# Kernel tuning notes

Measured on AMD Instinct MI355X. Metric: run time of the kernel, lower is better.

## Reference

```python
import jax, jax.numpy as jnp
import numpy as np

LATENT_DIM = 256
BOOK_SIZE = 8192


def setup_inputs() -> dict:
    key = jax.random.key(0)
    k1, k2 = jax.random.split(key)
    z_e = jax.random.normal(k1, (16, LATENT_DIM, 32, 32), dtype=jnp.float32)
    codebook = jax.random.normal(k2, (BOOK_SIZE, LATENT_DIM), dtype=jnp.float32)
    return {"z_e": z_e, "codebook": codebook}


def reference(z_e, codebook):
    # NCHW -> NHWC -> (B*H*W, D)
    flat_z = jnp.transpose(z_e, (0, 2, 3, 1)).reshape(-1, LATENT_DIM)
    # squared euclidean distance via matmul: ||z||^2 + ||e||^2 - 2 z.e
    dist = (
        jnp.sum(flat_z ** 2, axis=1, keepdims=True)
        + jnp.sum(codebook ** 2, axis=1)
        - 2.0 * flat_z @ codebook.T
    )  # (N, book_size)
    indices = jnp.argmin(dist, axis=1)          # (N,)
    z_q = codebook[indices]                      # (N, D) gather
    return z_q, indices
```

## Files before the change

kernel.cpp:

```cpp
#include <hip/hip_runtime.h>
#include <stdint.h>

#define NROWS 16384
#define NCODES 8192
#define DIM 256
#define EPS_S 0.4f
#define SM 0.8f

typedef __attribute__((ext_vector_type(8))) short bf16x8;
typedef __attribute__((ext_vector_type(16))) float f32x16;
typedef unsigned int uint32;

__device__ __forceinline__ unsigned short f2bf(float f) {
  union { float f; unsigned int u; } v; v.f = f;
  unsigned int u = v.u;
  return (unsigned short)((u + 0x7FFFu + ((u >> 16) & 1u)) >> 16);
}

__device__ __forceinline__ unsigned long long packdi(float d, int idx) {
  unsigned int u = __float_as_uint(d);
  u = (u & 0x80000000u) ? ~u : (u | 0x80000000u);
  return ((unsigned long long)u << 32) | (unsigned int)idx;
}
__device__ __forceinline__ unsigned long long u64min(unsigned long long a,
                                                     unsigned long long b) {
  return a < b ? a : b;
}
__device__ __forceinline__ unsigned long long shflx64(unsigned long long v, int m) {
  int lo = __shfl_xor((int)(unsigned int)v, m);
  int hi = __shfl_xor((int)(v >> 32), m);
  return ((unsigned long long)(unsigned int)hi << 32) | (unsigned int)lo;
}
__device__ __forceinline__ uint32 umax(uint32 a, uint32 b) { return a > b ? a : b; }
__device__ __forceinline__ uint32 umin(uint32 a, uint32 b) { return a < b ? a : b; }

__device__ __forceinline__ void glds16(const ushort* g, ushort* l) {
  __builtin_amdgcn_global_load_lds(
      (const __attribute__((address_space(1))) unsigned int*)g,
      (__attribute__((address_space(3))) unsigned int*)l, 16, 0, 0);
}

__global__ __launch_bounds__(256) void prep(const float* __restrict__ z,
                                            const float* __restrict__ cb,
                                            float* __restrict__ flatz,
                                            ushort* __restrict__ zb,
                                            ushort* __restrict__ eb,
                                            float* __restrict__ enorm) {
  __shared__ float t[32][33];
  const int blk = blockIdx.x;
  if (blk < 4096) {
    const int tx = threadIdx.x & 31, ty = threadIdx.x >> 5;
    const int ht = blk & 31, ct = (blk >> 5) & 7, b = blk >> 8;
    const float* src = z + (size_t)b * 262144 + (size_t)(ct * 32) * 1024 + ht * 32;
#pragma unroll
    for (int i = 0; i < 4; ++i) {
      int c = ty + i * 8;
      t[c][tx] = src[c * 1024 + tx];
    }
    __syncthreads();
#pragma unroll
    for (int i = 0; i < 4; ++i) {
      int hw = ty + i * 8;
      int row = b * 1024 + ht * 32 + hw;
      float v = t[tx][hw];
      flatz[(size_t)row * 256 + ct * 32 + tx] = v;
      zb[(size_t)row * 256 + ct * 32 + tx] = f2bf(v);
    }
  } else {
    const int lane = threadIdx.x & 63, wave = threadIdx.x >> 6;
    const int code = (blk - 4096) * 4 + wave;
    float4 v = *(const float4*)(cb + (size_t)code * 256 + lane * 4);
    ushort4 o;
    o.x = f2bf(v.x); o.y = f2bf(v.y); o.z = f2bf(v.z); o.w = f2bf(v.w);
    *(ushort4*)(eb + (size_t)code * 256 + lane * 4) = o;
    float ss = v.x * v.x + v.y * v.y + v.z * v.z + v.w * v.w;
#pragma unroll
    for (int s = 1; s < 64; s <<= 1) ss += __shfl_xor(ss, s);
    if (lane == 0) enorm[code] = ss;
  }
}

__device__ __forceinline__ void init_acc(f32x16 acc[4][2], const float* en,
                                         int ot, int wm, int lg) {
#pragma unroll
  for (int m = 0; m < 4; ++m) {
    const float* ep = en + ot * 256 + wm * 128 + m * 32 + 4 * lg;
    float4 e0 = *(const float4*)(ep);
    float4 e1 = *(const float4*)(ep + 8);
    float4 e2 = *(const float4*)(ep + 16);
    float4 e3 = *(const float4*)(ep + 24);
    f32x16 c0;
    c0[0]  = 1024.f - 0.5f * e0.x; c0[1]  = 1024.f - 0.5f * e0.y;
    c0[2]  = 1024.f - 0.5f * e0.z; c0[3]  = 1024.f - 0.5f * e0.w;
    c0[4]  = 1024.f - 0.5f * e1.x; c0[5]  = 1024.f - 0.5f * e1.y;
    c0[6]  = 1024.f - 0.5f * e1.z; c0[7]  = 1024.f - 0.5f * e1.w;
    c0[8]  = 1024.f - 0.5f * e2.x; c0[9]  = 1024.f - 0.5f * e2.y;
    c0[10] = 1024.f - 0.5f * e2.z; c0[11] = 1024.f - 0.5f * e2.w;
    c0[12] = 1024.f - 0.5f * e3.x; c0[13] = 1024.f - 0.5f * e3.y;
    c0[14] = 1024.f - 0.5f * e3.z; c0[15] = 1024.f - 0.5f * e3.w;
    acc[m][0] = c0; acc[m][1] = c0;
  }
}

__device__ __forceinline__ void epilogue(const f32x16 acc[4][2],
                                         uint32* __restrict__ bm, int cg,
                                         int ot, int zrow0, int wm, int wn,
                                         int l31, int lg) {
  const int cid0 = cg * 128 + ot * 16 + wm * 8;
#pragma unroll
  for (int n = 0; n < 2; ++n) {
    uint32 res[8];
#pragma unroll
    for (int m = 0; m < 4; ++m)
#pragma unroll
      for (int hc = 0; hc < 2; ++hc) {
        uint32 m1 = 0, m2 = 0;
#pragma unroll
        for (int p = 0; p < 8; ++p) {
          uint32 id = (uint32)((p & 3) | (lg << 2) | ((p >> 2) << 3));
          uint32 pv = (__float_as_uint(acc[m][n][hc * 8 + p]) & ~31u) | id;
          m2 = umax(m2, umin(m1, pv));
          m1 = umax(m1, pv);
        }
        uint32 o1 = (uint32)__shfl_xor((int)m1, 32);
        uint32 o2 = (uint32)__shfl_xor((int)m2, 32);
        m2 = umax(umax(m2, o2), umin(m1, o1));
        m1 = umax(m1, o1);
        float s1 = __uint_as_float(m1 & ~31u);
        float s2 = __uint_as_float(m2 & ~31u);
        res[m * 2 + hc] = (s1 - s2 > SM) ? (m1 | 16u) : m1;
      }
    const int zr = zrow0 + wn * 64 + n * 32 + l31;
    uint4 o;
    o.x = lg ? res[4] : res[0];
    o.y = lg ? res[5] : res[1];
    o.z = lg ? res[6] : res[2];
    o.w = lg ? res[7] : res[3];
    *(uint4*)(bm + (size_t)zr * 512 + cid0 + lg * 4) = o;
  }
}

__global__ __launch_bounds__(512, 2) void vq_gemm(const ushort* __restrict__ eb,
                                                  const ushort* __restrict__ zb,
                                                  const float* __restrict__ enorm,
                                                  uint32* __restrict__ bm) {
  __shared__ __align__(16) ushort As[4 * 8192];
  __shared__ __align__(16) ushort Bs[4 * 8192];
  __shared__ __align__(16) float en[2048];
  const int tid = threadIdx.x;
  const int wave = tid >> 6, lane = tid & 63;
  const int wm = wave >> 2, wn = wave & 3;
  const int l31 = lane & 31, lg = lane >> 5;
  const int y = blockIdx.x & 63, cg = blockIdx.x >> 6;
  const int code00 = cg * 2048;
  const int zrow0 = y * 256;

  *(float4*)&en[tid * 4] = *(const float4*)(enorm + code00 + tid * 4);
  __syncthreads();

  const int u0 = tid, u1 = tid + 512;
  const ushort* aU0 = eb + (size_t)(code00 + (u0 >> 2)) * 256 +
                      ((u0 & 3) ^ ((u0 >> 3) & 3)) * 8;
  const ushort* aU1 = eb + (size_t)(code00 + (u1 >> 2)) * 256 +
                      ((u1 & 3) ^ ((u1 >> 3) & 3)) * 8;
  const ushort* bU0 = zb + (size_t)(zrow0 + (u0 >> 2)) * 256 +
                      ((u0 & 3) ^ ((u0 >> 3) & 3)) * 8;
  const ushort* bU1 = zb + (size_t)(zrow0 + (u1 >> 2)) * 256 +
                      ((u1 & 3) ^ ((u1 >> 3) & 3)) * 8;
  ushort* aL = As + wave * 512;
  ushort* bL = Bs + wave * 512;

#pragma unroll
  for (int c = 0; c < 3; ++c) {
    glds16(aU0 + c * 32, aL + c * 8192);
    glds16(aU1 + c * 32, aL + c * 8192 + 4096);
    glds16(bU0 + c * 32, bL + c * 8192);
    glds16(bU1 + c * 32, bL + c * 8192 + 4096);
  }

  f32x16 acc[4][2];
  init_acc(acc, en, 0, wm, lg);

  asm volatile("s_waitcnt vmcnt(8)" ::: "memory");
  __builtin_amdgcn_s_barrier();
  asm volatile("" ::: "memory");

  const int swz = (l31 >> 1) & 3;
  const int colu0 = ((0 | lg) ^ swz) * 8;
  const int colu1 = ((2 | lg) ^ swz) * 8;
  const int arow_u = (wm * 128 + l31) * 32;
  const int brow_u = (wn * 64 + l31) * 32;

#pragma unroll 1
  for (int ot = 0; ot < 8; ++ot) {
    if (ot > 0) {
      epilogue(acc, bm, cg, ot - 1, zrow0, wm, wn, l31, lg);
      init_acc(acc, en, ot, wm, lg);
    }
#pragma unroll
    for (int cc = 0; cc < 8; ++cc) {
      const int slot = cc & 3;
      if (ot < 7 || cc <= 4) {
        const int s2 = (cc + 3) & 3;
        const size_t off = (size_t)((cc + 3) >> 3) * 65536 +
                           (size_t)ot * 65536 + ((cc + 3) & 7) * 32;
        const size_t boff = ((cc + 3) & 7) * 32;
        glds16(aU0 + off, aL + s2 * 8192);
        glds16(aU1 + off, aL + s2 * 8192 + 4096);
        glds16(bU0 + boff, bL + s2 * 8192);
        glds16(bU1 + boff, bL + s2 * 8192 + 4096);
      }
      bf16x8 a0[4], a1[4], b0[2], b1[2];
#pragma unroll
      for (int m = 0; m < 4; ++m) {
        a0[m] = *(const bf16x8*)&As[slot * 8192 + arow_u + m * 1024 + colu0];
        a1[m] = *(const bf16x8*)&As[slot * 8192 + arow_u + m * 1024 + colu1];
      }
#pragma unroll
      for (int n = 0; n < 2; ++n) {
        b0[n] = *(const bf16x8*)&Bs[slot * 8192 + brow_u + n * 1024 + colu0];
        b1[n] = *(const bf16x8*)&Bs[slot * 8192 + brow_u + n * 1024 + colu1];
      }
      __builtin_amdgcn_s_setprio(1);
#pragma unroll
      for (int m = 0; m < 4; ++m)
#pragma unroll
        for (int n = 0; n < 2; ++n)
          acc[m][n] = __builtin_amdgcn_mfma_f32_32x32x16_bf16(a0[m], b0[n],
                                                              acc[m][n], 0, 0, 0);
#pragma unroll
      for (int m = 0; m < 4; ++m)
#pragma unroll
        for (int n = 0; n < 2; ++n)
          acc[m][n] = __builtin_amdgcn_mfma_f32_32x32x16_bf16(a1[m], b1[n],
                                                              acc[m][n], 0, 0, 0);
      __builtin_amdgcn_s_setprio(0);
      if (ot < 7 || cc <= 4) {
        asm volatile("s_waitcnt vmcnt(8)" ::: "memory");
        __builtin_amdgcn_s_barrier();
        asm volatile("" ::: "memory");
      } else if (cc == 5) {
        asm volatile("s_waitcnt vmcnt(4)" ::: "memory");
        __builtin_amdgcn_s_barrier();
        asm volatile("" ::: "memory");
      } else if (cc == 6) {
        asm volatile("s_waitcnt vmcnt(0)" ::: "memory");
        __builtin_amdgcn_s_barrier();
        asm volatile("" ::: "memory");
      }
    }
  }
  epilogue(acc, bm, cg, 7, zrow0, wm, wn, l31, lg);
}

__device__ __forceinline__ unsigned long long chunk_exact(
    int chunk, const float* __restrict__ zrow, const float* __restrict__ cb,
    const float* __restrict__ enorm, int lane) {
  const int code = chunk * 16 + (lane >> 2);
  const float* zp = zrow + (lane & 3) * 64;
  const float* cp = cb + (size_t)code * 256 + (lane & 3) * 64;
  float s = 0.f;
#pragma unroll
  for (int d = 0; d < 64; d += 4) {
    float4 zv = *(const float4*)(zp + d);
    float4 cv = *(const float4*)(cp + d);
    s = fmaf(zv.x, cv.x, s); s = fmaf(zv.y, cv.y, s);
    s = fmaf(zv.z, cv.z, s); s = fmaf(zv.w, cv.w, s);
  }
  s += __shfl_xor(s, 1);
  s += __shfl_xor(s, 2);
  float dist = fmaf(-2.f, s, enorm[code]);
  unsigned long long key = ((lane & 3) == 0) ? packdi(dist, code) : ~0ull;
#pragma unroll
  for (int m = 1; m < 64; m <<= 1) key = u64min(key, shflx64(key, m));
  return key;
}

__global__ __launch_bounds__(256) void vq_sel(const uint32* __restrict__ bm,
                                              const float* __restrict__ flatz,
                                              const float* __restrict__ cb,
                                              const float* __restrict__ enorm,
                                              float* __restrict__ zq,
                                              float* __restrict__ oidx) {
  const int lane = threadIdx.x & 63;
  const int row = blockIdx.x * 4 + (threadIdx.x >> 6);
  uint4 va = *(const uint4*)(bm + (size_t)row * 512 + lane * 8);
  uint4 vb = *(const uint4*)(bm + (size_t)row * 512 + lane * 8 + 4);
  uint32 v[8] = {va.x, va.y, va.z, va.w, vb.x, vb.y, vb.z, vb.w};
  uint32 m1 = 0, m2 = 0; int ch = 0;
#pragma unroll
  for (int s = 0; s < 8; ++s) {
    uint32 pv = v[s];
    m2 = umax(m2, umin(m1, pv));
    ch = (pv > m1) ? (lane * 8 + s) : ch;
    m1 = umax(m1, pv);
  }
#pragma unroll
  for (int m = 1; m < 64; m <<= 1) {
    uint32 o1 = (uint32)__shfl_xor((int)m1, m);
    uint32 o2 = (uint32)__shfl_xor((int)m2, m);
    int oc = __shfl_xor(ch, m);
    m2 = umax(umax(m2, o2), umin(m1, o1));
    ch = (o1 > m1) ? oc : ch;
    m1 = umax(m1, o1);
  }
  float s1 = __uint_as_float(m1 & ~31u);
  float s2 = __uint_as_float(m2 & ~31u);
  int idx;
  if ((m1 & 16u) && (s1 - s2 > SM)) {
    idx = ch * 16 + (int)(m1 & 15u);
  } else {
    const float* zrow = flatz + (size_t)row * 256;
    unsigned long long key = chunk_exact(ch, zrow, cb, enorm, lane);
    float dbest;
    { unsigned int u = (unsigned int)(key >> 32);
      u = (u & 0x80000000u) ? (u & 0x7FFFFFFFu) : ~u;
      dbest = __uint_as_float(u); }
    float thr = (1024.f - 0.5f * dbest) - EPS_S;
#pragma unroll
    for (int s = 0; s < 8; ++s) {
      bool cand = __uint_as_float(v[s] & ~31u) >= thr;
      unsigned long long mk = __ballot(cand);
      while (mk) {
        int L = __ffsll(mk) - 1;
        mk &= mk - 1;
        int c2 = L * 8 + s;
        if (c2 == ch) continue;
        key = u64min(key, chunk_exact(c2, zrow, cb, enorm, lane));
      }
    }
    idx = (int)(key & 0xFFFFFFFFull);
  }
  if (lane == 0) oidx[row] = (float)idx;
  float4 val = *(const float4*)(cb + (size_t)idx * 256 + lane * 4);
  *(float4*)(zq + (size_t)row * 256 + lane * 4) = val;
}

extern "C" void kernel_launch(void* const* d_in, const int* in_sizes, int n_in,
                              void* d_out, int out_size, void* d_ws, size_t ws_size,
                              hipStream_t stream) {
  const float* z = (const float*)d_in[0];
  const float* cb = (const float*)d_in[1];
  char* ws = (char*)d_ws;
  ushort* zb = (ushort*)(ws);
  ushort* eb = (ushort*)(ws + (8u << 20));
  float* enorm = (float*)(ws + (12u << 20));
  uint32* bm = (uint32*)(ws + (13u << 20));
  float* zq = (float*)d_out;
  float* oidx = zq + (size_t)NROWS * DIM;
  float* flatz = zq;

  prep<<<4096 + NCODES / 4, 256, 0, stream>>>(z, cb, flatz, zb, eb, enorm);
  vq_gemm<<<256, 512, 0, stream>>>(eb, zb, enorm, bm);
  vq_sel<<<NROWS / 4, 256, 0, stream>>>(bm, flatz, cb, enorm, zq, oidx);
}
```

Before: 182.7 us.

## Hold z tile in registers and halve per-block code range to double grid

Each wave now loads its whole 64-row slice of the bf16 z tile (full K=256) into registers once, instead of streaming z through a shared-memory ring alongside the codebook. The B shared buffer and its global-to-LDS copies are removed, cutting LDS traffic and freeing LDS. Each block now covers 1024 codes instead of 2048 and the grid doubles to 512 blocks, which spreads work over more CUs. The cost is 64 extra VGPRs per lane for the z fragments, which risks spills or lower occupancy under the 512x2 launch bounds, and each z tile is now reloaded by twice as many blocks.

```diff
diff --git a/kernel.cpp b/kernel.cpp
--- a/kernel.cpp
+++ b/kernel.cpp
@@ -106,7 +106,7 @@
                                          uint32* __restrict__ bm, int cg,
                                          int ot, int zrow0, int wm, int wn,
                                          int l31, int lg) {
-  const int cid0 = cg * 128 + ot * 16 + wm * 8;
+  const int cid0 = cg * 64 + ot * 16 + wm * 8;
 #pragma unroll
   for (int n = 0; n < 2; ++n) {
     uint32 res[8];
@@ -145,43 +145,49 @@
                                                   const float* __restrict__ enorm,
                                                   uint32* __restrict__ bm) {
   __shared__ __align__(16) ushort As[4 * 8192];
-  __shared__ __align__(16) ushort Bs[4 * 8192];
-  __shared__ __align__(16) float en[2048];
+  __shared__ __align__(16) float en[1024];
   const int tid = threadIdx.x;
   const int wave = tid >> 6, lane = tid & 63;
   const int wm = wave >> 2, wn = wave & 3;
   const int l31 = lane & 31, lg = lane >> 5;
   const int y = blockIdx.x & 63, cg = blockIdx.x >> 6;
-  const int code00 = cg * 2048;
+  const int code00 = cg * 1024;
   const int zrow0 = y * 256;
 
-  *(float4*)&en[tid * 4] = *(const float4*)(enorm + code00 + tid * 4);
+  if (tid < 256)
+    *(float4*)&en[tid * 4] = *(const float4*)(enorm + code00 + tid * 4);
   __syncthreads();
+
+  bf16x8 breg[8][2][2];
+  {
+    const ushort* bbase = zb + (size_t)(zrow0 + wn * 64 + l31) * 256 + lg * 8;
+#pragma unroll
+    for (int cc = 0; cc < 8; ++cc)
+#pragma unroll
+      for (int ks = 0; ks < 2; ++ks)
+#pragma unroll
+        for (int n = 0; n < 2; ++n)
+          breg[cc][ks][n] =
+              *(const bf16x8*)(bbase + n * 8192 + cc * 32 + ks * 16);
+  }
 
   const int u0 = tid, u1 = tid + 512;
   const ushort* aU0 = eb + (size_t)(code00 + (u0 >> 2)) * 256 +
                       ((u0 & 3) ^ ((u0 >> 3) & 3)) * 8;
   const ushort* aU1 = eb + (size_t)(code00 + (u1 >> 2)) * 256 +
                       ((u1 & 3) ^ ((u1 >> 3) & 3)) * 8;
-  const ushort* bU0 = zb + (size_t)(zrow0 + (u0 >> 2)) * 256 +
-                      ((u0 & 3) ^ ((u0 >> 3) & 3)) * 8;
-  const ushort* bU1 = zb + (size_t)(zrow0 + (u1 >> 2)) * 256 +
-                      ((u1 & 3) ^ ((u1 >> 3) & 3)) * 8;
   ushort* aL = As + wave * 512;
-  ushort* bL = Bs + wave * 512;
 
 #pragma unroll
   for (int c = 0; c < 3; ++c) {
     glds16(aU0 + c * 32, aL + c * 8192);
     glds16(aU1 + c * 32, aL + c * 8192 + 4096);
-    glds16(bU0 + c * 32, bL + c * 8192);
-    glds16(bU1 + c * 32, bL + c * 8192 + 4096);
   }
 
   f32x16 acc[4][2];
   init_acc(acc, en, 0, wm, lg);
 
-  asm volatile("s_waitcnt vmcnt(8)" ::: "memory");
+  asm volatile("s_waitcnt vmcnt(4)" ::: "memory");
   __builtin_amdgcn_s_barrier();
   asm volatile("" ::: "memory");
 
@@ -189,10 +195,9 @@
   const int colu0 = ((0 | lg) ^ swz) * 8;
   const int colu1 = ((2 | lg) ^ swz) * 8;
   const int arow_u = (wm * 128 + l31) * 32;
-  const int brow_u = (wn * 64 + l31) * 32;
 
 #pragma unroll 1
-  for (int ot = 0; ot < 8; ++ot) {
+  for (int ot = 0; ot < 4; ++ot) {
     if (ot > 0) {
       epilogue(acc, bm, cg, ot - 1, zrow0, wm, wn, l31, lg);
       init_acc(acc, en, ot, wm, lg);
@@ -200,47 +205,39 @@
 #pragma unroll
     for (int cc = 0; cc < 8; ++cc) {
       const int slot = cc & 3;
-      if (ot < 7 || cc <= 4) {
-        const int s2 = (cc + 3) & 3;
-        const size_t off = (size_t)((cc + 3) >> 3) * 65536 +
-                           (size_t)ot * 65536 + ((cc + 3) & 7) * 32;
-        const size_t boff = ((cc + 3) & 7) * 32;
-        glds16(aU0 + off, aL + s2 * 8192);
-        glds16(aU1 + off, aL + s2 * 8192 + 4096);
-        glds16(bU0 + boff, bL + s2 * 8192);
-        glds16(bU1 + boff, bL + s2 * 8192 + 4096);
-      }
-      bf16x8 a0[4], a1[4], b0[2], b1[2];
+      bf16x8 a0[4], a1[4];
 #pragma unroll
       for (int m = 0; m < 4; ++m) {
         a0[m] = *(const bf16x8*)&As[slot * 8192 + arow_u + m * 1024 + colu0];
         a1[m] = *(const bf16x8*)&As[slot * 8192 + arow_u + m * 1024 + colu1];
       }
-#pragma unroll
-      for (int n = 0; n < 2; ++n) {
-        b0[n] = *(const bf16x8*)&Bs[slot * 8192 + brow_u + n * 1024 + colu0];
-        b1[n] = *(const bf16x8*)&Bs[slot * 8192 + brow_u + n * 1024 + colu1];
+      if (ot < 3 || cc <= 4) {
+        const int s2 = (cc + 3) & 3;
+        const size_t off = (size_t)(((cc + 3) >> 3) + ot) * 65536 +
+                           ((cc + 3) & 7) * 32;
+        glds16(aU0 + off, aL + s2 * 8192);
+        glds16(aU1 + off, aL + s2 * 8192 + 4096);
       }
       __builtin_amdgcn_s_setprio(1);
 #pragma unroll
       for (int m = 0; m < 4; ++m)
 #pragma unroll
         for (int n = 0; n < 2; ++n)
-          acc[m][n] = __builtin_amdgcn_mfma_f32_32x32x16_bf16(a0[m], b0[n],
-                                                              acc[m][n], 0, 0, 0);
+          acc[m][n] = __builtin_amdgcn_mfma_f32_32x32x16_bf16(
+              a0[m], breg[cc][0][n], acc[m][n], 0, 0, 0);
 #pragma unroll
       for (int m = 0; m < 4; ++m)
 #pragma unroll
         for (int n = 0; n < 2; ++n)
-          acc[m][n] = __builtin_amdgcn_mfma_f32_32x32x16_bf16(a1[m], b1[n],
-                                                              acc[m][n], 0, 0, 0);
+          acc[m][n] = __builtin_amdgcn_mfma_f32_32x32x16_bf16(
+              a1[m], breg[cc][1][n], acc[m][n], 0, 0, 0);
       __builtin_amdgcn_s_setprio(0);
-      if (ot < 7 || cc <= 4) {
-        asm volatile("s_waitcnt vmcnt(8)" ::: "memory");
+      if (ot < 3 || cc <= 4) {
+        asm volatile("s_waitcnt vmcnt(4)" ::: "memory");
         __builtin_amdgcn_s_barrier();
         asm volatile("" ::: "memory");
       } else if (cc == 5) {
-        asm volatile("s_waitcnt vmcnt(4)" ::: "memory");
+        asm volatile("s_waitcnt vmcnt(2)" ::: "memory");
         __builtin_amdgcn_s_barrier();
         asm volatile("" ::: "memory");
       } else if (cc == 6) {
@@ -250,7 +247,7 @@
       }
     }
   }
-  epilogue(acc, bm, cg, 7, zrow0, wm, wn, l31, lg);
+  epilogue(acc, bm, cg, 3, zrow0, wm, wn, l31, lg);
 }
 
 __device__ __forceinline__ unsigned long long chunk_exact(
@@ -351,6 +348,6 @@
   float* flatz = zq;
 
   prep<<<4096 + NCODES / 4, 256, 0, stream>>>(z, cb, flatz, zb, eb, enorm);
-  vq_gemm<<<256, 512, 0, stream>>>(eb, zb, enorm, bm);
+  vq_gemm<<<512, 512, 0, stream>>>(eb, zb, enorm, bm);
   vq_sel<<<NROWS / 4, 256, 0, stream>>>(bm, flatz, cb, enorm, zq, oidx);
 }
```

Measured after the change: 230.8 us. 1.26x slower.

## Rework GEMM K-tiling to double-buffered 64-wide tiles and split selection into worklist pass

Applied to the files above, without the earlier changes.

The GEMM main loop moves from a 4-slot ring of 32-wide K chunks to a 2-slot double buffer of 64-wide K chunks, with an 8-row XOR swizzle and A fragments loaded in two halves to limit register pressure. It now waits for all loads and syncs once per tile instead of per chunk. The selection kernel is split in two. A scan pass resolves confident rows immediately and appends ambiguous rows to an atomic worklist. A persistent exact-refinement kernel then pulls rows dynamically, to balance the uneven fallback work. The trade-off is an extra launch, atomics, and a full vmcnt(0) wait per tile, which may expose load latency.

```diff
diff --git a/kernel.cpp b/kernel.cpp
--- a/kernel.cpp
+++ b/kernel.cpp
@@ -45,9 +45,11 @@
                                             float* __restrict__ flatz,
                                             ushort* __restrict__ zb,
                                             ushort* __restrict__ eb,
-                                            float* __restrict__ enorm) {
+                                            float* __restrict__ enorm,
+                                            uint32* __restrict__ wl) {
   __shared__ float t[32][33];
   const int blk = blockIdx.x;
+  if (blk == 0 && threadIdx.x == 0) { wl[0] = 0u; wl[1] = 0u; }
   if (blk < 4096) {
     const int tx = threadIdx.x & 31, ty = threadIdx.x >> 5;
     const int ht = blk & 31, ct = (blk >> 5) & 7, b = blk >> 8;
@@ -144,8 +146,8 @@
                                                   const ushort* __restrict__ zb,
                                                   const float* __restrict__ enorm,
                                                   uint32* __restrict__ bm) {
-  __shared__ __align__(16) ushort As[4 * 8192];
-  __shared__ __align__(16) ushort Bs[4 * 8192];
+  __shared__ __align__(16) ushort As[2][16384];
+  __shared__ __align__(16) ushort Bs[2][16384];
   __shared__ __align__(16) float en[2048];
   const int tid = threadIdx.x;
   const int wave = tid >> 6, lane = tid & 63;
@@ -156,40 +158,30 @@
   const int zrow0 = y * 256;
 
   *(float4*)&en[tid * 4] = *(const float4*)(enorm + code00 + tid * 4);
+
+  const int srow = tid >> 3;
+  const int g = (tid & 7) ^ (srow & 7);
+  const ushort* aS = eb + (size_t)(code00 + srow) * 256 + g * 8;
+  const ushort* bS = zb + (size_t)(zrow0 + srow) * 256 + g * 8;
+  const int ldst = wave * 512;
+
+#pragma unroll
+  for (int j = 0; j < 4; ++j) glds16(aS + j * 16384, &As[0][ldst + j * 4096]);
+#pragma unroll
+  for (int j = 0; j < 4; ++j) glds16(bS + j * 16384, &Bs[0][ldst + j * 4096]);
+
+  asm volatile("s_waitcnt vmcnt(0)" ::: "memory");
   __syncthreads();
-
-  const int u0 = tid, u1 = tid + 512;
-  const ushort* aU0 = eb + (size_t)(code00 + (u0 >> 2)) * 256 +
-                      ((u0 & 3) ^ ((u0 >> 3) & 3)) * 8;
-  const ushort* aU1 = eb + (size_t)(code00 + (u1 >> 2)) * 256 +
-                      ((u1 & 3) ^ ((u1 >> 3) & 3)) * 8;
-  const ushort* bU0 = zb + (size_t)(zrow0 + (u0 >> 2)) * 256 +
-                      ((u0 & 3) ^ ((u0 >> 3) & 3)) * 8;
-  const ushort* bU1 = zb + (size_t)(zrow0 + (u1 >> 2)) * 256 +
-                      ((u1 & 3) ^ ((u1 >> 3) & 3)) * 8;
-  ushort* aL = As + wave * 512;
-  ushort* bL = Bs + wave * 512;
-
-#pragma unroll
-  for (int c = 0; c < 3; ++c) {
-    glds16(aU0 + c * 32, aL + c * 8192);
-    glds16(aU1 + c * 32, aL + c * 8192 + 4096);
-    glds16(bU0 + c * 32, bL + c * 8192);
-    glds16(bU1 + c * 32, bL + c * 8192 + 4096);
-  }
 
   f32x16 acc[4][2];
   init_acc(acc, en, 0, wm, lg);
 
-  asm volatile("s_waitcnt vmcnt(8)" ::: "memory");
-  __builtin_amdgcn_s_barrier();
-  asm volatile("" ::: "memory");
-
-  const int swz = (l31 >> 1) & 3;
-  const int colu0 = ((0 | lg) ^ swz) * 8;
-  const int colu1 = ((2 | lg) ^ swz) * 8;
-  const int arow_u = (wm * 128 + l31) * 32;
-  const int brow_u = (wn * 64 + l31) * 32;
+  const int swz = l31 & 7;
+  int col[4];
+#pragma unroll
+  for (int ks = 0; ks < 4; ++ks) col[ks] = (((ks * 2) | lg) ^ swz) * 8;
+  const int arow = (wm * 128 + l31) * 64;
+  const int brow = (wn * 64 + l31) * 64;
 
 #pragma unroll 1
   for (int ot = 0; ot < 8; ++ot) {
@@ -198,52 +190,57 @@
       init_acc(acc, en, ot, wm, lg);
     }
 #pragma unroll
-    for (int cc = 0; cc < 8; ++cc) {
-      const int slot = cc & 3;
-      if (ot < 7 || cc <= 4) {
-        const int s2 = (cc + 3) & 3;
-        const size_t off = (size_t)((cc + 3) >> 3) * 65536 +
-                           (size_t)ot * 65536 + ((cc + 3) & 7) * 32;
-        const size_t boff = ((cc + 3) & 7) * 32;
-        glds16(aU0 + off, aL + s2 * 8192);
-        glds16(aU1 + off, aL + s2 * 8192 + 4096);
-        glds16(bU0 + boff, bL + s2 * 8192);
-        glds16(bU1 + boff, bL + s2 * 8192 + 4096);
-      }
-      bf16x8 a0[4], a1[4], b0[2], b1[2];
-#pragma unroll
-      for (int m = 0; m < 4; ++m) {
-        a0[m] = *(const bf16x8*)&As[slot * 8192 + arow_u + m * 1024 + colu0];
-        a1[m] = *(const bf16x8*)&As[slot * 8192 + arow_u + m * 1024 + colu1];
-      }
-#pragma unroll
-      for (int n = 0; n < 2; ++n) {
-        b0[n] = *(const bf16x8*)&Bs[slot * 8192 + brow_u + n * 1024 + colu0];
-        b1[n] = *(const bf16x8*)&Bs[slot * 8192 + brow_u + n * 1024 + colu1];
+    for (int kt = 0; kt < 4; ++kt) {
+      const int tt = ot * 4 + kt;
+      const int s = tt & 1;
+      bf16x8 a[2][4], b[2][4];
+#pragma unroll
+      for (int mi = 0; mi < 2; ++mi)
+#pragma unroll
+        for (int ks = 0; ks < 4; ++ks)
+          a[mi][ks] = *(const bf16x8*)&As[s][arow + mi * 2048 + col[ks]];
+#pragma unroll
+      for (int n = 0; n < 2; ++n)
+#pragma unroll
+        for (int ks = 0; ks < 4; ++ks)
+          b[n][ks] = *(const bf16x8*)&Bs[s][brow + n * 2048 + col[ks]];
+      if (tt <= 30) {
+        const int tn = tt + 1;
+        const size_t ao = (size_t)(tn >> 2) * 65536 + (size_t)(tn & 3) * 64;
+        const size_t bo = (size_t)(tn & 3) * 64;
+        ushort* aD = &As[tn & 1][ldst];
+        ushort* bD = &Bs[tn & 1][ldst];
+#pragma unroll
+        for (int j = 0; j < 4; ++j) glds16(aS + j * 16384 + ao, aD + j * 4096);
+#pragma unroll
+        for (int j = 0; j < 4; ++j) glds16(bS + j * 16384 + bo, bD + j * 4096);
       }
       __builtin_amdgcn_s_setprio(1);
 #pragma unroll
-      for (int m = 0; m < 4; ++m)
-#pragma unroll
-        for (int n = 0; n < 2; ++n)
-          acc[m][n] = __builtin_amdgcn_mfma_f32_32x32x16_bf16(a0[m], b0[n],
-                                                              acc[m][n], 0, 0, 0);
-#pragma unroll
-      for (int m = 0; m < 4; ++m)
-#pragma unroll
-        for (int n = 0; n < 2; ++n)
-          acc[m][n] = __builtin_amdgcn_mfma_f32_32x32x16_bf16(a1[m], b1[n],
-                                                              acc[m][n], 0, 0, 0);
+      for (int ks = 0; ks < 4; ++ks)
+#pragma unroll
+        for (int mi = 0; mi < 2; ++mi)
+#pragma unroll
+          for (int n = 0; n < 2; ++n)
+            acc[mi][n] = __builtin_amdgcn_mfma_f32_32x32x16_bf16(
+                a[mi][ks], b[n][ks], acc[mi][n], 0, 0, 0);
       __builtin_amdgcn_s_setprio(0);
-      if (ot < 7 || cc <= 4) {
-        asm volatile("s_waitcnt vmcnt(8)" ::: "memory");
-        __builtin_amdgcn_s_barrier();
-        asm volatile("" ::: "memory");
-      } else if (cc == 5) {
-        asm volatile("s_waitcnt vmcnt(4)" ::: "memory");
-        __builtin_amdgcn_s_barrier();
-        asm volatile("" ::: "memory");
-      } else if (cc == 6) {
+#pragma unroll
+      for (int mi = 0; mi < 2; ++mi)
+#pragma unroll
+        for (int ks = 0; ks < 4; ++ks)
+          a[mi][ks] = *(const bf16x8*)&As[s][arow + (2 + mi) * 2048 + col[ks]];
+      __builtin_amdgcn_s_setprio(1);
+#pragma unroll
+      for (int ks = 0; ks < 4; ++ks)
+#pragma unroll
+        for (int mi = 0; mi < 2; ++mi)
+#pragma unroll
+          for (int n = 0; n < 2; ++n)
+            acc[2 + mi][n] = __builtin_amdgcn_mfma_f32_32x32x16_bf16(
+                a[mi][ks], b[n][ks], acc[2 + mi][n], 0, 0, 0);
+      __builtin_amdgcn_s_setprio(0);
+      if (tt <= 30) {
         asm volatile("s_waitcnt vmcnt(0)" ::: "memory");
         __builtin_amdgcn_s_barrier();
         asm volatile("" ::: "memory");
@@ -276,17 +273,13 @@
   return key;
 }
 
-__global__ __launch_bounds__(256) void vq_sel(const uint32* __restrict__ bm,
-                                              const float* __restrict__ flatz,
-                                              const float* __restrict__ cb,
-                                              const float* __restrict__ enorm,
-                                              float* __restrict__ zq,
-                                              float* __restrict__ oidx) {
-  const int lane = threadIdx.x & 63;
-  const int row = blockIdx.x * 4 + (threadIdx.x >> 6);
+__device__ __forceinline__ void row_scan(const uint32* __restrict__ bm, int row,
+                                         int lane, uint32 v[8], uint32& m1o,
+                                         uint32& m2o, int& cho) {
   uint4 va = *(const uint4*)(bm + (size_t)row * 512 + lane * 8);
   uint4 vb = *(const uint4*)(bm + (size_t)row * 512 + lane * 8 + 4);
-  uint32 v[8] = {va.x, va.y, va.z, va.w, vb.x, vb.y, vb.z, vb.w};
+  v[0] = va.x; v[1] = va.y; v[2] = va.z; v[3] = va.w;
+  v[4] = vb.x; v[5] = vb.y; v[6] = vb.z; v[7] = vb.w;
   uint32 m1 = 0, m2 = 0; int ch = 0;
 #pragma unroll
   for (int s = 0; s < 8; ++s) {
@@ -304,12 +297,50 @@
     ch = (o1 > m1) ? oc : ch;
     m1 = umax(m1, o1);
   }
+  m1o = m1; m2o = m2; cho = ch;
+}
+
+__global__ __launch_bounds__(256) void vq_scan(const uint32* __restrict__ bm,
+                                               const float* __restrict__ cb,
+                                               float* __restrict__ zq,
+                                               float* __restrict__ oidx,
+                                               uint32* __restrict__ wl) {
+  const int lane = threadIdx.x & 63;
+  const int row = blockIdx.x * 4 + (threadIdx.x >> 6);
+  uint32 v[8], m1, m2; int ch;
+  row_scan(bm, row, lane, v, m1, m2, ch);
   float s1 = __uint_as_float(m1 & ~31u);
   float s2 = __uint_as_float(m2 & ~31u);
-  int idx;
   if ((m1 & 16u) && (s1 - s2 > SM)) {
-    idx = ch * 16 + (int)(m1 & 15u);
+    int idx = ch * 16 + (int)(m1 & 15u);
+    if (lane == 0) oidx[row] = (float)idx;
+    float4 val = *(const float4*)(cb + (size_t)idx * 256 + lane * 4);
+    *(float4*)(zq + (size_t)row * 256 + lane * 4) = val;
   } else {
+    if (lane == 0) {
+      uint32 p = atomicAdd(wl, 1u);
+      wl[2 + p] = (uint32)row;
+    }
+  }
+}
+
+__global__ __launch_bounds__(256) void vq_exact(const uint32* __restrict__ bm,
+                                                const float* __restrict__ flatz,
+                                                const float* __restrict__ cb,
+                                                const float* __restrict__ enorm,
+                                                float* __restrict__ zq,
+                                                float* __restrict__ oidx,
+                                                uint32* __restrict__ wl) {
+  const int lane = threadIdx.x & 63;
+  const uint32 total = wl[0];
+  for (;;) {
+    int t = 0;
+    if (lane == 0) t = (int)atomicAdd(wl + 1, 1u);
+    t = __shfl(t, 0);
+    if ((uint32)t >= total) break;
+    const int row = (int)wl[2 + t];
+    uint32 v[8], m1, m2; int ch;
+    row_scan(bm, row, lane, v, m1, m2, ch);
     const float* zrow = flatz + (size_t)row * 256;
     unsigned long long key = chunk_exact(ch, zrow, cb, enorm, lane);
     float dbest;
@@ -329,11 +360,11 @@
         key = u64min(key, chunk_exact(c2, zrow, cb, enorm, lane));
       }
     }
-    idx = (int)(key & 0xFFFFFFFFull);
-  }
-  if (lane == 0) oidx[row] = (float)idx;
-  float4 val = *(const float4*)(cb + (size_t)idx * 256 + lane * 4);
-  *(float4*)(zq + (size_t)row * 256 + lane * 4) = val;
+    int idx = (int)(key & 0xFFFFFFFFull);
+    if (lane == 0) oidx[row] = (float)idx;
+    float4 val = *(const float4*)(cb + (size_t)idx * 256 + lane * 4);
+    *(float4*)(zq + (size_t)row * 256 + lane * 4) = val;
+  }
 }
 
 extern "C" void kernel_launch(void* const* d_in, const int* in_sizes, int n_in,
@@ -345,12 +376,14 @@
   ushort* zb = (ushort*)(ws);
   ushort* eb = (ushort*)(ws + (8u << 20));
   float* enorm = (float*)(ws + (12u << 20));
+  uint32* wl = (uint32*)(ws + (12u << 20) + (64u << 10));
   uint32* bm = (uint32*)(ws + (13u << 20));
   float* zq = (float*)d_out;
   float* oidx = zq + (size_t)NROWS * DIM;
   float* flatz = zq;
 
-  prep<<<4096 + NCODES / 4, 256, 0, stream>>>(z, cb, flatz, zb, eb, enorm);
+  prep<<<4096 + NCODES / 4, 256, 0, stream>>>(z, cb, flatz, zb, eb, enorm, wl);
   vq_gemm<<<256, 512, 0, stream>>>(eb, zb, enorm, bm);
-  vq_sel<<<NROWS / 4, 256, 0, stream>>>(bm, flatz, cb, enorm, zq, oidx);
-}
+  vq_scan<<<NROWS / 4, 256, 0, stream>>>(bm, cb, zq, oidx, wl);
+  vq_exact<<<256, 256, 0, stream>>>(bm, flatz, cb, enorm, zq, oidx, wl);
+}
```

Result: slower. 246.0 us (+34.6%).

## Shrink GEMM tiles to 128x256, double-buffer, and grid-stride prep and select kernels

Applied to the files above, without the earlier changes.

The distance GEMM block tile is halved in both rows and codes, and the launch grows to four times as many blocks with a higher occupancy hint. The four-stage LDS pipeline becomes a simple double buffer with a full wait each step. The prep and selection kernels are changed to loop over several work items per block with fewer blocks. The aim is better CU occupancy and load balance, at the cost of less operand reuse per block and a shallower load pipeline.

```diff
diff --git a/kernel.cpp b/kernel.cpp
--- a/kernel.cpp
+++ b/kernel.cpp
@@ -47,44 +47,48 @@
                                             ushort* __restrict__ eb,
                                             float* __restrict__ enorm) {
   __shared__ float t[32][33];
-  const int blk = blockIdx.x;
-  if (blk < 4096) {
-    const int tx = threadIdx.x & 31, ty = threadIdx.x >> 5;
-    const int ht = blk & 31, ct = (blk >> 5) & 7, b = blk >> 8;
-    const float* src = z + (size_t)b * 262144 + (size_t)(ct * 32) * 1024 + ht * 32;
-#pragma unroll
-    for (int i = 0; i < 4; ++i) {
-      int c = ty + i * 8;
-      t[c][tx] = src[c * 1024 + tx];
+#pragma unroll 1
+  for (int it = 0; it < 4; ++it) {
+    const int blk = blockIdx.x + it * 1536;
+    if (blk < 4096) {
+      const int tx = threadIdx.x & 31, ty = threadIdx.x >> 5;
+      const int ht = blk & 31, ct = (blk >> 5) & 7, b = blk >> 8;
+      const float* src = z + (size_t)b * 262144 + (size_t)(ct * 32) * 1024 + ht * 32;
+#pragma unroll
+      for (int i = 0; i < 4; ++i) {
+        int c = ty + i * 8;
+        t[c][tx] = src[c * 1024 + tx];
+      }
+      __syncthreads();
+#pragma unroll
+      for (int i = 0; i < 4; ++i) {
+        int hw = ty + i * 8;
+        int row = b * 1024 + ht * 32 + hw;
+        float v = t[tx][hw];
+        flatz[(size_t)row * 256 + ct * 32 + tx] = v;
+        zb[(size_t)row * 256 + ct * 32 + tx] = f2bf(v);
+      }
+    } else {
+      const int lane = threadIdx.x & 63, wave = threadIdx.x >> 6;
+      const int code = (blk - 4096) * 4 + wave;
+      float4 v = *(const float4*)(cb + (size_t)code * 256 + lane * 4);
+      ushort4 o;
+      o.x = f2bf(v.x); o.y = f2bf(v.y); o.z = f2bf(v.z); o.w = f2bf(v.w);
+      *(ushort4*)(eb + (size_t)code * 256 + lane * 4) = o;
+      float ss = v.x * v.x + v.y * v.y + v.z * v.z + v.w * v.w;
+#pragma unroll
+      for (int s = 1; s < 64; s <<= 1) ss += __shfl_xor(ss, s);
+      if (lane == 0) enorm[code] = ss;
     }
     __syncthreads();
-#pragma unroll
-    for (int i = 0; i < 4; ++i) {
-      int hw = ty + i * 8;
-      int row = b * 1024 + ht * 32 + hw;
-      float v = t[tx][hw];
-      flatz[(size_t)row * 256 + ct * 32 + tx] = v;
-      zb[(size_t)row * 256 + ct * 32 + tx] = f2bf(v);
-    }
-  } else {
-    const int lane = threadIdx.x & 63, wave = threadIdx.x >> 6;
-    const int code = (blk - 4096) * 4 + wave;
-    float4 v = *(const float4*)(cb + (size_t)code * 256 + lane * 4);
-    ushort4 o;
-    o.x = f2bf(v.x); o.y = f2bf(v.y); o.z = f2bf(v.z); o.w = f2bf(v.w);
-    *(ushort4*)(eb + (size_t)code * 256 + lane * 4) = o;
-    float ss = v.x * v.x + v.y * v.y + v.z * v.z + v.w * v.w;
-#pragma unroll
-    for (int s = 1; s < 64; s <<= 1) ss += __shfl_xor(ss, s);
-    if (lane == 0) enorm[code] = ss;
-  }
-}
-
-__device__ __forceinline__ void init_acc(f32x16 acc[4][2], const float* en,
+  }
+}
+
+__device__ __forceinline__ void init_acc(f32x16 acc[2][2], const float* en,
                                          int ot, int wm, int lg) {
 #pragma unroll
-  for (int m = 0; m < 4; ++m) {
-    const float* ep = en + ot * 256 + wm * 128 + m * 32 + 4 * lg;
+  for (int m = 0; m < 2; ++m) {
+    const float* ep = en + ot * 256 + wm * 64 + m * 32 + 4 * lg;
     float4 e0 = *(const float4*)(ep);
     float4 e1 = *(const float4*)(ep + 8);
     float4 e2 = *(const float4*)(ep + 16);
@@ -102,16 +106,16 @@
   }
 }
 
-__device__ __forceinline__ void epilogue(const f32x16 acc[4][2],
+__device__ __forceinline__ void epilogue(const f32x16 acc[2][2],
                                          uint32* __restrict__ bm, int cg,
                                          int ot, int zrow0, int wm, int wn,
                                          int l31, int lg) {
-  const int cid0 = cg * 128 + ot * 16 + wm * 8;
+  const int cid0 = cg * 64 + ot * 16 + wm * 4;
 #pragma unroll
   for (int n = 0; n < 2; ++n) {
-    uint32 res[8];
-#pragma unroll
-    for (int m = 0; m < 4; ++m)
+    uint32 res[4];
+#pragma unroll
+    for (int m = 0; m < 2; ++m)
 #pragma unroll
       for (int hc = 0; hc < 2; ++hc) {
         uint32 m1 = 0, m2 = 0;
@@ -131,32 +135,30 @@
         res[m * 2 + hc] = (s1 - s2 > SM) ? (m1 | 16u) : m1;
       }
     const int zr = zrow0 + wn * 64 + n * 32 + l31;
-    uint4 o;
-    o.x = lg ? res[4] : res[0];
-    o.y = lg ? res[5] : res[1];
-    o.z = lg ? res[6] : res[2];
-    o.w = lg ? res[7] : res[3];
-    *(uint4*)(bm + (size_t)zr * 512 + cid0 + lg * 4) = o;
-  }
-}
-
-__global__ __launch_bounds__(512, 2) void vq_gemm(const ushort* __restrict__ eb,
+    if (lg == 0) {
+      uint4 o; o.x = res[0]; o.y = res[1]; o.z = res[2]; o.w = res[3];
+      *(uint4*)(bm + (size_t)zr * 512 + cid0) = o;
+    }
+  }
+}
+
+__global__ __launch_bounds__(512, 4) void vq_gemm(const ushort* __restrict__ eb,
                                                   const ushort* __restrict__ zb,
                                                   const float* __restrict__ enorm,
                                                   uint32* __restrict__ bm) {
-  __shared__ __align__(16) ushort As[4 * 8192];
-  __shared__ __align__(16) ushort Bs[4 * 8192];
-  __shared__ __align__(16) float en[2048];
+  __shared__ __align__(16) ushort As[2 * 8192];
+  __shared__ __align__(16) ushort Bs[2 * 4096];
+  __shared__ __align__(16) float en[1024];
   const int tid = threadIdx.x;
   const int wave = tid >> 6, lane = tid & 63;
-  const int wm = wave >> 2, wn = wave & 3;
+  const int wm = wave >> 1, wn = wave & 1;
   const int l31 = lane & 31, lg = lane >> 5;
-  const int y = blockIdx.x & 63, cg = blockIdx.x >> 6;
-  const int code00 = cg * 2048;
-  const int zrow0 = y * 256;
-
-  *(float4*)&en[tid * 4] = *(const float4*)(enorm + code00 + tid * 4);
-  __syncthreads();
+  const int y = blockIdx.x & 127, cg = blockIdx.x >> 7;
+  const int code00 = cg * 1024;
+  const int zrow0 = y * 128;
+
+  if (tid < 256)
+    *(float4*)&en[tid * 4] = *(const float4*)(enorm + code00 + tid * 4);
 
   const int u0 = tid, u1 = tid + 512;
   const ushort* aU0 = eb + (size_t)(code00 + (u0 >> 2)) * 256 +
@@ -165,92 +167,75 @@
                       ((u1 & 3) ^ ((u1 >> 3) & 3)) * 8;
   const ushort* bU0 = zb + (size_t)(zrow0 + (u0 >> 2)) * 256 +
                       ((u0 & 3) ^ ((u0 >> 3) & 3)) * 8;
-  const ushort* bU1 = zb + (size_t)(zrow0 + (u1 >> 2)) * 256 +
-                      ((u1 & 3) ^ ((u1 >> 3) & 3)) * 8;
-  ushort* aL = As + wave * 512;
-  ushort* bL = Bs + wave * 512;
-
-#pragma unroll
-  for (int c = 0; c < 3; ++c) {
-    glds16(aU0 + c * 32, aL + c * 8192);
-    glds16(aU1 + c * 32, aL + c * 8192 + 4096);
-    glds16(bU0 + c * 32, bL + c * 8192);
-    glds16(bU1 + c * 32, bL + c * 8192 + 4096);
-  }
-
-  f32x16 acc[4][2];
+  const int aL = wave * 512;
+
+  glds16(aU0, As + aL);
+  glds16(aU1, As + aL + 4096);
+  glds16(bU0, Bs + aL);
+
+  asm volatile("s_waitcnt vmcnt(0)" ::: "memory");
+  __syncthreads();
+
+  f32x16 acc[2][2];
   init_acc(acc, en, 0, wm, lg);
-
-  asm volatile("s_waitcnt vmcnt(8)" ::: "memory");
-  __builtin_amdgcn_s_barrier();
-  asm volatile("" ::: "memory");
 
   const int swz = (l31 >> 1) & 3;
   const int colu0 = ((0 | lg) ^ swz) * 8;
   const int colu1 = ((2 | lg) ^ swz) * 8;
-  const int arow_u = (wm * 128 + l31) * 32;
+  const int arow_u = (wm * 64 + l31) * 32;
   const int brow_u = (wn * 64 + l31) * 32;
 
 #pragma unroll 1
-  for (int ot = 0; ot < 8; ++ot) {
+  for (int ot = 0; ot < 4; ++ot) {
     if (ot > 0) {
       epilogue(acc, bm, cg, ot - 1, zrow0, wm, wn, l31, lg);
       init_acc(acc, en, ot, wm, lg);
     }
 #pragma unroll
-    for (int cc = 0; cc < 8; ++cc) {
-      const int slot = cc & 3;
-      if (ot < 7 || cc <= 4) {
-        const int s2 = (cc + 3) & 3;
-        const size_t off = (size_t)((cc + 3) >> 3) * 65536 +
-                           (size_t)ot * 65536 + ((cc + 3) & 7) * 32;
-        const size_t boff = ((cc + 3) & 7) * 32;
-        glds16(aU0 + off, aL + s2 * 8192);
-        glds16(aU1 + off, aL + s2 * 8192 + 4096);
-        glds16(bU0 + boff, bL + s2 * 8192);
-        glds16(bU1 + boff, bL + s2 * 8192 + 4096);
-      }
-      bf16x8 a0[4], a1[4], b0[2], b1[2];
-#pragma unroll
-      for (int m = 0; m < 4; ++m) {
-        a0[m] = *(const bf16x8*)&As[slot * 8192 + arow_u + m * 1024 + colu0];
-        a1[m] = *(const bf16x8*)&As[slot * 8192 + arow_u + m * 1024 + colu1];
+    for (int kc = 0; kc < 8; ++kc) {
+      const int c = ot * 8 + kc;
+      const int s = c & 1, sn = s ^ 1;
+      if (c < 31) {
+        const int cn = c + 1;
+        const size_t ao = (size_t)(cn >> 3) * 65536 + (size_t)(cn & 7) * 32;
+        const size_t bo = (size_t)(cn & 7) * 32;
+        glds16(aU0 + ao, As + sn * 8192 + aL);
+        glds16(aU1 + ao, As + sn * 8192 + aL + 4096);
+        glds16(bU0 + bo, Bs + sn * 4096 + aL);
+      }
+      bf16x8 a0[2], a1[2], b0[2], b1[2];
+#pragma unroll
+      for (int m = 0; m < 2; ++m) {
+        a0[m] = *(const bf16x8*)&As[s * 8192 + arow_u + m * 1024 + colu0];
+        a1[m] = *(const bf16x8*)&As[s * 8192 + arow_u + m * 1024 + colu1];
       }
 #pragma unroll
       for (int n = 0; n < 2; ++n) {
-        b0[n] = *(const bf16x8*)&Bs[slot * 8192 + brow_u + n * 1024 + colu0];
-        b1[n] = *(const bf16x8*)&Bs[slot * 8192 + brow_u + n * 1024 + colu1];
+        b0[n] = *(const bf16x8*)&Bs[s * 4096 + brow_u + n * 1024 + colu0];
+        b1[n] = *(const bf16x8*)&Bs[s * 4096 + brow_u + n * 1024 + colu1];
       }
       __builtin_amdgcn_s_setprio(1);
 #pragma unroll
-      for (int m = 0; m < 4; ++m)
+      for (int m = 0; m < 2; ++m)
 #pragma unroll
         for (int n = 0; n < 2; ++n)
           acc[m][n] = __builtin_amdgcn_mfma_f32_32x32x16_bf16(a0[m], b0[n],
                                                               acc[m][n], 0, 0, 0);
 #pragma unroll
-      for (int m = 0; m < 4; ++m)
+      for (int m = 0; m < 2; ++m)
 #pragma unroll
         for (int n = 0; n < 2; ++n)
           acc[m][n] = __builtin_amdgcn_mfma_f32_32x32x16_bf16(a1[m], b1[n],
                                                               acc[m][n], 0, 0, 0);
       __builtin_amdgcn_s_setprio(0);
-      if (ot < 7 || cc <= 4) {
-        asm volatile("s_waitcnt vmcnt(8)" ::: "memory");
-        __builtin_amdgcn_s_barrier();
-        asm volatile("" ::: "memory");
-      } else if (cc == 5) {
-        asm volatile("s_waitcnt vmcnt(4)" ::: "memory");
-        __builtin_amdgcn_s_barrier();
-        asm volatile("" ::: "memory");
-      } else if (cc == 6) {
+      if (c < 31) {
         asm volatile("s_waitcnt vmcnt(0)" ::: "memory");
         __builtin_amdgcn_s_barrier();
         asm volatile("" ::: "memory");
       }
     }
   }
-  epilogue(acc, bm, cg, 7, zrow0, wm, wn, l31, lg);
+  epilogue(acc, bm, cg, 3, zrow0, wm, wn, l31, lg);
 }
 
 __device__ __forceinline__ unsigned long long chunk_exact(
@@ -283,57 +268,60 @@
                                               float* __restrict__ zq,
                                               float* __restrict__ oidx) {
   const int lane = threadIdx.x & 63;
-  const int row = blockIdx.x * 4 + (threadIdx.x >> 6);
-  uint4 va = *(const uint4*)(bm + (size_t)row * 512 + lane * 8);
-  uint4 vb = *(const uint4*)(bm + (size_t)row * 512 + lane * 8 + 4);
-  uint32 v[8] = {va.x, va.y, va.z, va.w, vb.x, vb.y, vb.z, vb.w};
-  uint32 m1 = 0, m2 = 0; int ch = 0;
-#pragma unroll
-  for (int s = 0; s < 8; ++s) {
-    uint32 pv = v[s];
-    m2 = umax(m2, umin(m1, pv));
-    ch = (pv > m1) ? (lane * 8 + s) : ch;
-    m1 = umax(m1, pv);
-  }
-#pragma unroll
-  for (int m = 1; m < 64; m <<= 1) {
-    uint32 o1 = (uint32)__shfl_xor((int)m1, m);
-    uint32 o2 = (uint32)__shfl_xor((int)m2, m);
-    int oc = __shfl_xor(ch, m);
-    m2 = umax(umax(m2, o2), umin(m1, o1));
-    ch = (o1 > m1) ? oc : ch;
-    m1 = umax(m1, o1);
-  }
-  float s1 = __uint_as_float(m1 & ~31u);
-  float s2 = __uint_as_float(m2 & ~31u);
-  int idx;
-  if ((m1 & 16u) && (s1 - s2 > SM)) {
-    idx = ch * 16 + (int)(m1 & 15u);
-  } else {
-    const float* zrow = flatz + (size_t)row * 256;
-    unsigned long long key = chunk_exact(ch, zrow, cb, enorm, lane);
-    float dbest;
-    { unsigned int u = (unsigned int)(key >> 32);
-      u = (u & 0x80000000u) ? (u & 0x7FFFFFFFu) : ~u;
-      dbest = __uint_as_float(u); }
-    float thr = (1024.f - 0.5f * dbest) - EPS_S;
+#pragma unroll 1
+  for (int it = 0; it < 4; ++it) {
+    const int row = blockIdx.x * 16 + it * 4 + (threadIdx.x >> 6);
+    uint4 va = *(const uint4*)(bm + (size_t)row * 512 + lane * 8);
+    uint4 vb = *(const uint4*)(bm + (size_t)row * 512 + lane * 8 + 4);
+    uint32 v[8] = {va.x, va.y, va.z, va.w, vb.x, vb.y, vb.z, vb.w};
+    uint32 m1 = 0, m2 = 0; int ch = 0;
 #pragma unroll
     for (int s = 0; s < 8; ++s) {
-      bool cand = __uint_as_float(v[s] & ~31u) >= thr;
-      unsigned long long mk = __ballot(cand);
-      while (mk) {
-        int L = __ffsll(mk) - 1;
-        mk &= mk - 1;
-        int c2 = L * 8 + s;
-        if (c2 == ch) continue;
-        key = u64min(key, chunk_exact(c2, zrow, cb, enorm, lane));
-      }
-    }
-    idx = (int)(key & 0xFFFFFFFFull);
-  }
-  if (lane == 0) oidx[row] = (float)idx;
-  float4 val = *(const float4*)(cb + (size_t)idx * 256 + lane * 4);
-  *(float4*)(zq + (size_t)row * 256 + lane * 4) = val;
+      uint32 pv = v[s];
+      m2 = umax(m2, umin(m1, pv));
+      ch = (pv > m1) ? (lane * 8 + s) : ch;
+      m1 = umax(m1, pv);
+    }
+#pragma unroll
+    for (int m = 1; m < 64; m <<= 1) {
+      uint32 o1 = (uint32)__shfl_xor((int)m1, m);
+      uint32 o2 = (uint32)__shfl_xor((int)m2, m);
+      int oc = __shfl_xor(ch, m);
+      m2 = umax(umax(m2, o2), umin(m1, o1));
+      ch = (o1 > m1) ? oc : ch;
+      m1 = umax(m1, o1);
+    }
+    float s1 = __uint_as_float(m1 & ~31u);
+    float s2 = __uint_as_float(m2 & ~31u);
+    int idx;
+    if ((m1 & 16u) && (s1 - s2 > SM)) {
+      idx = ch * 16 + (int)(m1 & 15u);
+    } else {
+      const float* zrow = flatz + (size_t)row * 256;
+      unsigned long long key = chunk_exact(ch, zrow, cb, enorm, lane);
+      float dbest;
+      { unsigned int u = (unsigned int)(key >> 32);
+        u = (u & 0x80000000u) ? (u & 0x7FFFFFFFu) : ~u;
+        dbest = __uint_as_float(u); }
+      float thr = (1024.f - 0.5f * dbest) - EPS_S;
+#pragma unroll
+      for (int s = 0; s < 8; ++s) {
+        bool cand = __uint_as_float(v[s] & ~31u) >= thr;
+        unsigned long long mk = __ballot(cand);
+        while (mk) {
+          int L = __ffsll(mk) - 1;
+          mk &= mk - 1;
+          int c2 = L * 8 + s;
+          if (c2 == ch) continue;
+          key = u64min(key, chunk_exact(c2, zrow, cb, enorm, lane));
+        }
+      }
+      idx = (int)(key & 0xFFFFFFFFull);
+    }
+    if (lane == 0) oidx[row] = (float)idx;
+    float4 val = *(const float4*)(cb + (size_t)idx * 256 + lane * 4);
+    *(float4*)(zq + (size_t)row * 256 + lane * 4) = val;
+  }
 }
 
 extern "C" void kernel_launch(void* const* d_in, const int* in_sizes, int n_in,
@@ -350,7 +338,7 @@
   float* oidx = zq + (size_t)NROWS * DIM;
   float* flatz = zq;
 
-  prep<<<4096 + NCODES / 4, 256, 0, stream>>>(z, cb, flatz, zb, eb, enorm);
-  vq_gemm<<<256, 512, 0, stream>>>(eb, zb, enorm, bm);
-  vq_sel<<<NROWS / 4, 256, 0, stream>>>(bm, flatz, cb, enorm, zq, oidx);
-}
+  prep<<<1536, 256, 0, stream>>>(z, cb, flatz, zb, eb, enorm);
+  vq_gemm<<<1024, 512, 0, stream>>>(eb, zb, enorm, bm);
+  vq_sel<<<1024, 256, 0, stream>>>(bm, flatz, cb, enorm, zq, oidx);
+}
```

Measured after the change: 216.5 us. +18.5%, slower.
